# Performance work log

Hardware: AMD Instinct MI355X
Metric: run time of the kernel (lower is better)

Reference implementation:

```python
import jax, jax.numpy as jnp
import numpy as np

B, L, D, NC, H = 2, 192, 768, 4, 256  # batch, seq_len, bert_hidden, num_case(+coref), hidden


def setup_inputs() -> dict:
    key = jax.random.key(0)
    ks = jax.random.split(key, 9)
    s = 0.02  # init scale
    return {
        "sequence_output": jax.random.normal(ks[0], (B, L, D), dtype=jnp.float32),
        "base_score": jax.random.normal(ks[1], (B, L, NC, L), dtype=jnp.float32),
        "Wp": jax.random.normal(ks[2], (D, H), dtype=jnp.float32) * s,
        "bp": jnp.zeros((H,), dtype=jnp.float32),
        "Wa": jax.random.normal(ks[3], (D, NC * H), dtype=jnp.float32) * s,
        "ba": jnp.zeros((NC * H,), dtype=jnp.float32),
        "Wmid": jax.random.normal(ks[4], (NC, H + NC, H), dtype=jnp.float32) * s,
        "bmid": jnp.zeros((NC, H), dtype=jnp.float32),
        "Wout": jax.random.normal(ks[5], (NC, H), dtype=jnp.float32) * s,
    }


def reference(sequence_output, base_score, Wp, bp, Wa, ba, Wmid, bmid, Wout):
    b, l, d = sequence_output.shape
    nc = Wmid.shape[0]
    h = Wp.shape[1]
    # dropout is identity in eval mode
    h_p = sequence_output @ Wp + bp                       # [B, L, H] (predicate)
    h_a = (sequence_output @ Wa + ba).reshape(b, l, nc, h)  # [B, L, NC, H] (argument)
    # broadcast add: predicate axis p, argument axis a -> [B, P, A, NC, H]
    h_pa = jnp.tanh(h_p[:, :, None, None, :] + h_a[:, None, :, :, :])
    # base_score [B, L, NC, L] -> transpose(2,3) -> [B, P, A, NC], expand over case axis
    bs = jnp.swapaxes(base_score, 2, 3)                   # [B, P, A, NC]
    bs = jnp.broadcast_to(bs[:, :, :, None, :], (b, l, l, nc, nc))
    hcat = jnp.concatenate([h_pa, bs], axis=-1)           # [B, P, A, NC, H+NC]
    # per-case mid Linear, batched as a single einsum over the case axis n
    h_mid = jnp.tanh(jnp.einsum('bpanc,nch->bpanh', hcat, Wmid) + bmid)
    out = jnp.einsum('bpanh,nh->bpan', h_mid, Wout)       # [B, P, A, NC]
    return jnp.transpose(out, (0, 1, 3, 2))               # [B, P, NC, A]
```

## Files before the change

kernel.cpp:

```cpp
#include <hip/hip_runtime.h>

#define LSEQ 192
#define DIM  768
#define NCASE 4
#define HID  256
#define BATCH 2

#define TANH_K 2.885390081777927f

typedef float  floatx4 __attribute__((ext_vector_type(4)));
typedef __bf16 bf16x8  __attribute__((ext_vector_type(8)));

__device__ __forceinline__ float tanh_pre(float x) {
    float e = __builtin_amdgcn_exp2f(x);
    return 1.0f - 2.0f * __builtin_amdgcn_rcpf(e + 1.0f);
}

__device__ __forceinline__ void barrier_lds_only() {
    __builtin_amdgcn_sched_barrier(0);
    __builtin_amdgcn_s_waitcnt(0xC07F);
    __builtin_amdgcn_s_barrier();
    __builtin_amdgcn_sched_barrier(0);
}

template <int CTRL>
__device__ __forceinline__ float dpp_add(float v) {
    int x = __builtin_amdgcn_update_dpp(0, __builtin_bit_cast(int, v),
                                        CTRL, 0xF, 0xF, true);
    return v + __builtin_bit_cast(float, x);
}
__device__ __forceinline__ float row16_reduce(float v) {
    v = dpp_add<0xB1>(v);
    v = dpp_add<0x4E>(v);
    v = dpp_add<0x141>(v);
    v = dpp_add<0x140>(v);
    return v;
}


__global__ __launch_bounds__(256) void prep(
    const float* __restrict__ seq, const float* __restrict__ Wp,
    const float* __restrict__ Wa,  const float* __restrict__ bp,
    const float* __restrict__ ba,  const float* __restrict__ Wmid,
    const float* __restrict__ bmid,
    float* __restrict__ lin, bf16x8* __restrict__ Bpack)
{
    const int blk = blockIdx.x;
    const int tid = threadIdx.x;

    if (blk >= 480) {
        int u = (blk - 480) * 256 + tid;
        int lane = u & 63, f = u >> 6;
        int ct = f & 15, nk = f >> 4;
        int kc = nk % 9, n = nk / 9;
        int h = ct * 16 + (lane & 15);
        int kbase = kc * 32 + ((lane >> 4) & 3) * 8;
        bf16x8 v;
        #pragma unroll
        for (int j = 0; j < 8; j++) {
            int k = kbase + j;
            float x;
            if (k < 260)       x = Wmid[(size_t)(n * 260 + k) * 256 + h];
            else if (k == 260) x = bmid[n * 256 + h];
            else               x = 0.0f;
            v[j] = (__bf16)(TANH_K * x);
        }
        Bpack[u] = v;
        return;
    }

    const int w = tid >> 6, lane = tid & 63;
    const int u = blk * 4 + w;
    const int rt = u / 80, cg = u % 80;
    const int quad  = lane >> 4;
    const int col16 = lane & 15;

    const int arow = rt * 16 + col16;
    const int col  = cg * 16 + col16;
    const float* aptr = seq + (size_t)arow * DIM + quad * 8;
    const float* wbase = (cg < 16) ? (Wp + col) : (Wa + (col - 256));
    const int    wstr  = (cg < 16) ? HID : (NCASE * HID);

    floatx4 acc = {};
    floatx4 a0 = *(const floatx4*)(aptr);
    floatx4 a1 = *(const floatx4*)(aptr + 4);
    float bv[8];
    #pragma unroll
    for (int j = 0; j < 8; j++) bv[j] = wbase[(size_t)(quad * 8 + j) * wstr];

    #pragma unroll
    for (int kc = 0; kc < 24; kc++) {
        bf16x8 ah, al, bh, bl;
        #pragma unroll
        for (int j = 0; j < 4; j++) {
            __bf16 h0 = (__bf16)a0[j];
            ah[j] = h0; al[j] = (__bf16)(a0[j] - (float)h0);
            __bf16 h1 = (__bf16)a1[j];
            ah[4 + j] = h1; al[4 + j] = (__bf16)(a1[j] - (float)h1);
        }
        #pragma unroll
        for (int j = 0; j < 8; j++) {
            __bf16 h = (__bf16)bv[j];
            bh[j] = h; bl[j] = (__bf16)(bv[j] - (float)h);
        }
        if (kc < 23) {
            a0 = *(const floatx4*)(aptr + (kc + 1) * 32);
            a1 = *(const floatx4*)(aptr + (kc + 1) * 32 + 4);
            #pragma unroll
            for (int j = 0; j < 8; j++)
                bv[j] = wbase[(size_t)((kc + 1) * 32 + quad * 8 + j) * wstr];
        }
        acc = __builtin_amdgcn_mfma_f32_16x16x32_bf16(ah, bh, acc, 0, 0, 0);
        acc = __builtin_amdgcn_mfma_f32_16x16x32_bf16(al, bh, acc, 0, 0, 0);
        acc = __builtin_amdgcn_mfma_f32_16x16x32_bf16(ah, bl, acc, 0, 0, 0);
    }
    const float bias = (cg < 16) ? bp[col] : ba[col - 256];
    #pragma unroll
    for (int reg = 0; reg < 4; reg++)
        lin[(size_t)(rt * 16 + quad * 4 + reg) * 1280 + col] =
            TANH_K * (acc[reg] + bias);
}

__global__ __launch_bounds__(256, 2) void refine_main(
    const float* __restrict__ lin,
    const float* __restrict__ base_score,
    const float* __restrict__ Wout,
    const bf16x8* __restrict__ Bpack,
    float* __restrict__ out)
{
    const int bx = blockIdx.x;
    const int n  = blockIdx.y;
    const int b  = blockIdx.z;
    const int ptile = bx / 24, atile = bx % 24;
    const int p0 = ptile * 8, a0 = atile * 8;

    const int tid   = threadIdx.x;
    const int w     = tid >> 6;
    const int lane  = tid & 63;
    const int quad  = lane >> 4;
    const int col16 = lane & 15;

    __shared__ __align__(16) __bf16 A0[256 * 8];
    __shared__ __align__(16) __bf16 A1[256 * 8];
    __shared__ float red[4][64];

    const int row_gen = w * 16 + col16;
    const int pg = p0 + (row_gen >> 3), ag = a0 + (row_gen & 7);
    const float* hp_ptr = lin + (size_t)(b * LSEQ + pg) * 1280 + quad * 8;
    const float* ha_ptr = lin + (size_t)(b * LSEQ + ag) * 1280 + 256 + n * 256 + quad * 8;

    const bf16x8* bbase = Bpack + ((size_t)(n * 9) * 16 + w * 4) * 64 + lane;

    float bs4[4], wo[4];
    #pragma unroll
    for (int j = 0; j < 4; j++)
        bs4[j] = base_score[((size_t)(b * LSEQ + pg) * NCASE + j) * LSEQ + ag];
    #pragma unroll
    for (int ct = 0; ct < 4; ct++)
        wo[ct] = Wout[n * 256 + w * 64 + ct * 16 + col16];

    bf16x8 bcur[4];
    #pragma unroll
    for (int ct = 0; ct < 4; ct++) bcur[ct] = bbase[ct * 64];

    floatx4 hp0 = *(const floatx4*)(hp_ptr);
    floatx4 hp1 = *(const floatx4*)(hp_ptr + 4);
    floatx4 ha0 = *(const floatx4*)(ha_ptr);
    floatx4 ha1 = *(const floatx4*)(ha_ptr + 4);
    {
        floatx4 s0 = hp0 + ha0, s1 = hp1 + ha1;
        bf16x8 av;
        #pragma unroll
        for (int j = 0; j < 4; j++) {
            av[j]     = (__bf16)tanh_pre(s0[j]);
            av[4 + j] = (__bf16)tanh_pre(s1[j]);
        }
        *(bf16x8*)&A0[tid * 8] = av;
    }
    hp0 = *(const floatx4*)(hp_ptr + 32);
    hp1 = *(const floatx4*)(hp_ptr + 36);
    ha0 = *(const floatx4*)(ha_ptr + 32);
    ha1 = *(const floatx4*)(ha_ptr + 36);
    barrier_lds_only();

    floatx4 acc[4][4] = {};

    #pragma unroll
    for (int kc = 0; kc < 9; kc++) {
        bf16x8 bnext[4];
        if (kc < 8) {
            #pragma unroll
            for (int ct = 0; ct < 4; ct++)
                bnext[ct] = bbase[((kc + 1) * 16 + ct) * 64];
        }
        if (kc < 7) {
            floatx4 s0 = hp0 + ha0, s1 = hp1 + ha1;
            if (kc < 6) {
                hp0 = *(const floatx4*)(hp_ptr + (kc + 2) * 32);
                hp1 = *(const floatx4*)(hp_ptr + (kc + 2) * 32 + 4);
                ha0 = *(const floatx4*)(ha_ptr + (kc + 2) * 32);
                ha1 = *(const floatx4*)(ha_ptr + (kc + 2) * 32 + 4);
            }
            bf16x8 av;
            #pragma unroll
            for (int j = 0; j < 4; j++) {
                av[j]     = (__bf16)tanh_pre(s0[j]);
                av[4 + j] = (__bf16)tanh_pre(s1[j]);
            }
            __bf16* buf = ((kc + 1) & 1) ? A1 : A0;
            *(bf16x8*)&buf[tid * 8] = av;
        } else if (kc == 7) {
            bf16x8 av = {};
            if (quad == 0) {
                #pragma unroll
                for (int j = 0; j < 4; j++) av[j] = (__bf16)bs4[j];
                av[4] = (__bf16)1.0f;
            }
            *(bf16x8*)&A0[tid * 8] = av;
        }

        const __bf16* rb = (kc & 1) ? A1 : A0;
        bf16x8 af[4];
        #pragma unroll
        for (int rt = 0; rt < 4; rt++)
            af[rt] = *(const bf16x8*)&rb[(rt * 64 + lane) * 8];
        #pragma unroll
        for (int rt = 0; rt < 4; rt++)
            #pragma unroll
            for (int ct = 0; ct < 4; ct++)
                acc[rt][ct] = __builtin_amdgcn_mfma_f32_16x16x32_bf16(
                    af[rt], bcur[ct], acc[rt][ct], 0, 0, 0);
        #pragma unroll
        for (int ct = 0; ct < 4; ct++) bcur[ct] = bnext[ct];
        if (kc < 8) barrier_lds_only();
    }

    #pragma unroll
    for (int rt = 0; rt < 4; rt++) {
        #pragma unroll
        for (int reg = 0; reg < 4; reg++) {
            float rs = 0.0f;
            #pragma unroll
            for (int ct = 0; ct < 4; ct++)
                rs += tanh_pre(acc[rt][ct][reg]) * wo[ct];
            rs = row16_reduce(rs);
            if (col16 == 0) red[w][rt * 16 + quad * 4 + reg] = rs;
        }
    }
    barrier_lds_only();

    if (tid < 64) {
        float total = red[0][tid] + red[1][tid] + red[2][tid] + red[3][tid];
        const int p = p0 + (tid >> 3), a = a0 + (tid & 7);
        out[((size_t)(b * LSEQ + p) * NCASE + n) * LSEQ + a] = total;
    }
}

extern "C" void kernel_launch(void* const* d_in, const int* in_sizes, int n_in,
                              void* d_out, int out_size, void* d_ws, size_t ws_size,
                              hipStream_t stream) {
    const float* seq  = (const float*)d_in[0];
    const float* bsc  = (const float*)d_in[1];
    const float* Wp   = (const float*)d_in[2];
    const float* bp   = (const float*)d_in[3];
    const float* Wa   = (const float*)d_in[4];
    const float* ba   = (const float*)d_in[5];
    const float* Wmid = (const float*)d_in[6];
    const float* bmid = (const float*)d_in[7];
    const float* Wout = (const float*)d_in[8];
    float* out = (float*)d_out;

    char* ws = (char*)d_ws;
    float*  lin   = (float*)(ws);
    bf16x8* Bpack = (bf16x8*)(ws + 1966080);

    prep<<<624, 256, 0, stream>>>(seq, Wp, Wa, bp, ba, Wmid, bmid, lin, Bpack);
    refine_main<<<dim3(576, NCASE, BATCH), 256, 0, stream>>>(
        lin, bsc, Wout, Bpack, out);
}
```

Before: 151.8 us.

## Precompute tanh of projections and use tanh addition identity; enlarge main tile

The prep kernel now stores tanh of the predicate and argument projections, and splits its K loop across four waves with an LDS reduction. The main kernel then builds tanh(u+v) as (tu+tv)/(1+tu*tv), replacing an exp2 plus reciprocal per element with an FMA plus reciprocal. refine_main moves to 512-thread blocks covering 16 predicate rows, so each loaded Bpack fragment serves twice as many rows. In exchange it uses more LDS and larger blocks, which may reduce occupancy, and adds a little bf16 rounding difference from the identity.

```diff
diff --git a/kernel.cpp b/kernel.cpp
--- a/kernel.cpp
+++ b/kernel.cpp
@@ -10,10 +10,16 @@
 
 typedef float  floatx4 __attribute__((ext_vector_type(4)));
 typedef __bf16 bf16x8  __attribute__((ext_vector_type(8)));
+typedef __bf16 bf16x4  __attribute__((ext_vector_type(4)));
 
 __device__ __forceinline__ float tanh_pre(float x) {
     float e = __builtin_amdgcn_exp2f(x);
     return 1.0f - 2.0f * __builtin_amdgcn_rcpf(e + 1.0f);
+}
+
+__device__ __forceinline__ float tanh_add(float tu, float tv) {
+    float den = __builtin_fmaf(tu, tv, 1.0f);
+    return (tu + tv) * __builtin_amdgcn_rcpf(den);
 }
 
 __device__ __forceinline__ void barrier_lds_only() {
@@ -48,8 +54,8 @@
     const int blk = blockIdx.x;
     const int tid = threadIdx.x;
 
-    if (blk >= 480) {
-        int u = (blk - 480) * 256 + tid;
+    if (blk >= 1920) {
+        int u = (blk - 1920) * 256 + tid;
         int lane = u & 63, f = u >> 6;
         int ct = f & 15, nk = f >> 4;
         int kc = nk % 9, n = nk / 9;
@@ -70,14 +76,16 @@
     }
 
     const int w = tid >> 6, lane = tid & 63;
-    const int u = blk * 4 + w;
-    const int rt = u / 80, cg = u % 80;
+    const int rt = blk / 80, cg = blk % 80;
     const int quad  = lane >> 4;
     const int col16 = lane & 15;
 
+    __shared__ float cmb[3][256];
+
     const int arow = rt * 16 + col16;
     const int col  = cg * 16 + col16;
-    const float* aptr = seq + (size_t)arow * DIM + quad * 8;
+    const int kofs = w * 192;
+    const float* aptr = seq + (size_t)arow * DIM + kofs + quad * 8;
     const float* wbase = (cg < 16) ? (Wp + col) : (Wa + (col - 256));
     const int    wstr  = (cg < 16) ? HID : (NCASE * HID);
 
@@ -86,10 +94,11 @@
     floatx4 a1 = *(const floatx4*)(aptr + 4);
     float bv[8];
     #pragma unroll
-    for (int j = 0; j < 8; j++) bv[j] = wbase[(size_t)(quad * 8 + j) * wstr];
-
-    #pragma unroll
-    for (int kc = 0; kc < 24; kc++) {
+    for (int j = 0; j < 8; j++)
+        bv[j] = wbase[(size_t)(kofs + quad * 8 + j) * wstr];
+
+    #pragma unroll
+    for (int kc = 0; kc < 6; kc++) {
         bf16x8 ah, al, bh, bl;
         #pragma unroll
         for (int j = 0; j < 4; j++) {
@@ -103,25 +112,35 @@
             __bf16 h = (__bf16)bv[j];
             bh[j] = h; bl[j] = (__bf16)(bv[j] - (float)h);
         }
-        if (kc < 23) {
+        if (kc < 5) {
             a0 = *(const floatx4*)(aptr + (kc + 1) * 32);
             a1 = *(const floatx4*)(aptr + (kc + 1) * 32 + 4);
             #pragma unroll
             for (int j = 0; j < 8; j++)
-                bv[j] = wbase[(size_t)((kc + 1) * 32 + quad * 8 + j) * wstr];
+                bv[j] = wbase[(size_t)(kofs + (kc + 1) * 32 + quad * 8 + j) * wstr];
         }
         acc = __builtin_amdgcn_mfma_f32_16x16x32_bf16(ah, bh, acc, 0, 0, 0);
         acc = __builtin_amdgcn_mfma_f32_16x16x32_bf16(al, bh, acc, 0, 0, 0);
         acc = __builtin_amdgcn_mfma_f32_16x16x32_bf16(ah, bl, acc, 0, 0, 0);
     }
-    const float bias = (cg < 16) ? bp[col] : ba[col - 256];
-    #pragma unroll
-    for (int reg = 0; reg < 4; reg++)
-        lin[(size_t)(rt * 16 + quad * 4 + reg) * 1280 + col] =
-            TANH_K * (acc[reg] + bias);
-}
-
-__global__ __launch_bounds__(256, 2) void refine_main(
+
+    if (w > 0) *(floatx4*)&cmb[w - 1][lane * 4] = acc;
+    __syncthreads();
+    if (w == 0) {
+        #pragma unroll
+        for (int i = 0; i < 3; i++) {
+            floatx4 p = *(const floatx4*)&cmb[i][lane * 4];
+            acc += p;
+        }
+        const float bias = (cg < 16) ? bp[col] : ba[col - 256];
+        #pragma unroll
+        for (int reg = 0; reg < 4; reg++)
+            lin[(size_t)(rt * 16 + quad * 4 + reg) * 1280 + col] =
+                tanh_pre(TANH_K * (acc[reg] + bias));
+    }
+}
+
+__global__ __launch_bounds__(512, 4) void refine_main(
     const float* __restrict__ lin,
     const float* __restrict__ base_score,
     const float* __restrict__ Wout,
@@ -132,32 +151,37 @@
     const int n  = blockIdx.y;
     const int b  = blockIdx.z;
     const int ptile = bx / 24, atile = bx % 24;
-    const int p0 = ptile * 8, a0 = atile * 8;
+    const int p0 = ptile * 16, a0r = atile * 8;
 
     const int tid   = threadIdx.x;
     const int w     = tid >> 6;
     const int lane  = tid & 63;
     const int quad  = lane >> 4;
     const int col16 = lane & 15;
-
-    __shared__ __align__(16) __bf16 A0[256 * 8];
-    __shared__ __align__(16) __bf16 A1[256 * 8];
-    __shared__ float red[4][64];
+    const int rh    = w >> 2;
+    const int cq    = w & 3;
+
+    __shared__ __align__(16) __bf16 A0[512 * 8];
+    __shared__ __align__(16) __bf16 A1[512 * 8];
+    __shared__ float red[4][128];
 
     const int row_gen = w * 16 + col16;
-    const int pg = p0 + (row_gen >> 3), ag = a0 + (row_gen & 7);
+    const int pg = p0 + (row_gen >> 3), ag = a0r + (row_gen & 7);
     const float* hp_ptr = lin + (size_t)(b * LSEQ + pg) * 1280 + quad * 8;
     const float* ha_ptr = lin + (size_t)(b * LSEQ + ag) * 1280 + 256 + n * 256 + quad * 8;
 
-    const bf16x8* bbase = Bpack + ((size_t)(n * 9) * 16 + w * 4) * 64 + lane;
-
-    float bs4[4], wo[4];
-    #pragma unroll
-    for (int j = 0; j < 4; j++)
-        bs4[j] = base_score[((size_t)(b * LSEQ + pg) * NCASE + j) * LSEQ + ag];
+    const bf16x8* bbase = Bpack + ((size_t)(n * 9) * 16 + cq * 4) * 64 + lane;
+
+    float bs4[4] = {};
+    if (quad == 0) {
+        #pragma unroll
+        for (int j = 0; j < 4; j++)
+            bs4[j] = base_score[((size_t)(b * LSEQ + pg) * NCASE + j) * LSEQ + ag];
+    }
+    float wo[4];
     #pragma unroll
     for (int ct = 0; ct < 4; ct++)
-        wo[ct] = Wout[n * 256 + w * 64 + ct * 16 + col16];
+        wo[ct] = Wout[n * 256 + cq * 64 + ct * 16 + col16];
 
     bf16x8 bcur[4];
     #pragma unroll
@@ -168,12 +192,11 @@
     floatx4 ha0 = *(const floatx4*)(ha_ptr);
     floatx4 ha1 = *(const floatx4*)(ha_ptr + 4);
     {
-        floatx4 s0 = hp0 + ha0, s1 = hp1 + ha1;
         bf16x8 av;
         #pragma unroll
         for (int j = 0; j < 4; j++) {
-            av[j]     = (__bf16)tanh_pre(s0[j]);
-            av[4 + j] = (__bf16)tanh_pre(s1[j]);
+            av[j]     = (__bf16)tanh_add(hp0[j], ha0[j]);
+            av[4 + j] = (__bf16)tanh_add(hp1[j], ha1[j]);
         }
         *(bf16x8*)&A0[tid * 8] = av;
     }
@@ -194,7 +217,7 @@
                 bnext[ct] = bbase[((kc + 1) * 16 + ct) * 64];
         }
         if (kc < 7) {
-            floatx4 s0 = hp0 + ha0, s1 = hp1 + ha1;
+            floatx4 u0 = hp0, u1 = hp1, v0 = ha0, v1 = ha1;
             if (kc < 6) {
                 hp0 = *(const floatx4*)(hp_ptr + (kc + 2) * 32);
                 hp1 = *(const floatx4*)(hp_ptr + (kc + 2) * 32 + 4);
@@ -204,8 +227,8 @@
             bf16x8 av;
             #pragma unroll
             for (int j = 0; j < 4; j++) {
-                av[j]     = (__bf16)tanh_pre(s0[j]);
-                av[4 + j] = (__bf16)tanh_pre(s1[j]);
+                av[j]     = (__bf16)tanh_add(u0[j], v0[j]);
+                av[4 + j] = (__bf16)tanh_add(u1[j], v1[j]);
             }
             __bf16* buf = ((kc + 1) & 1) ? A1 : A0;
             *(bf16x8*)&buf[tid * 8] = av;
@@ -222,36 +245,37 @@
         const __bf16* rb = (kc & 1) ? A1 : A0;
         bf16x8 af[4];
         #pragma unroll
-        for (int rt = 0; rt < 4; rt++)
-            af[rt] = *(const bf16x8*)&rb[(rt * 64 + lane) * 8];
-        #pragma unroll
-        for (int rt = 0; rt < 4; rt++)
+        for (int rloc = 0; rloc < 4; rloc++)
+            af[rloc] = *(const bf16x8*)&rb[((rh * 4 + rloc) * 64 + lane) * 8];
+        #pragma unroll
+        for (int rloc = 0; rloc < 4; rloc++)
             #pragma unroll
             for (int ct = 0; ct < 4; ct++)
-                acc[rt][ct] = __builtin_amdgcn_mfma_f32_16x16x32_bf16(
-                    af[rt], bcur[ct], acc[rt][ct], 0, 0, 0);
+                acc[rloc][ct] = __builtin_amdgcn_mfma_f32_16x16x32_bf16(
+                    af[rloc], bcur[ct], acc[rloc][ct], 0, 0, 0);
         #pragma unroll
         for (int ct = 0; ct < 4; ct++) bcur[ct] = bnext[ct];
         if (kc < 8) barrier_lds_only();
     }
 
     #pragma unroll
-    for (int rt = 0; rt < 4; rt++) {
+    for (int rloc = 0; rloc < 4; rloc++) {
         #pragma unroll
         for (int reg = 0; reg < 4; reg++) {
             float rs = 0.0f;
             #pragma unroll
             for (int ct = 0; ct < 4; ct++)
-                rs += tanh_pre(acc[rt][ct][reg]) * wo[ct];
+                rs += tanh_pre(acc[rloc][ct][reg]) * wo[ct];
             rs = row16_reduce(rs);
-            if (col16 == 0) red[w][rt * 16 + quad * 4 + reg] = rs;
+            if (col16 == 0)
+                red[cq][rh * 64 + rloc * 16 + quad * 4 + reg] = rs;
         }
     }
     barrier_lds_only();
 
-    if (tid < 64) {
+    if (tid < 128) {
         float total = red[0][tid] + red[1][tid] + red[2][tid] + red[3][tid];
-        const int p = p0 + (tid >> 3), a = a0 + (tid & 7);
+        const int p = p0 + (tid >> 3), a = a0r + (tid & 7);
         out[((size_t)(b * LSEQ + p) * NCASE + n) * LSEQ + a] = total;
     }
 }
@@ -274,7 +298,7 @@
     float*  lin   = (float*)(ws);
     bf16x8* Bpack = (bf16x8*)(ws + 1966080);
 
-    prep<<<624, 256, 0, stream>>>(seq, Wp, Wa, bp, ba, Wmid, bmid, lin, Bpack);
-    refine_main<<<dim3(576, NCASE, BATCH), 256, 0, stream>>>(
+    prep<<<2064, 256, 0, stream>>>(seq, Wp, Wa, bp, ba, Wmid, bmid, lin, Bpack);
+    refine_main<<<dim3(288, NCASE, BATCH), 512, 0, stream>>>(
         lin, bsc, Wout, Bpack, out);
 }
```

Result: slower. 196.0 us (+29.1%).
